# Performance work log

Hardware: AMD Instinct MI355X
Metric: run time of the kernel (lower is better)

Reference implementation:

```python
import jax, jax.numpy as jnp
import numpy as np

N = 131072          # flattened ray-sample points
C = 32              # output_coordinate_dim per plane
BASE = 128          # base grid resolution
SCALES = [1, 2, 4]  # multiscale_res multipliers
HID = 256           # ResBlock / CondMLP hidden width
OUT = 16            # decoder output dim (geo features)
COMBS = [(0, 1), (0, 2), (1, 2)]  # itertools.combinations(range(3), 2)


def setup_inputs() -> dict:
    key = jax.random.key(0)
    ks = iter(jax.random.split(key, 64))
    inp = {}
    inp['pts'] = jax.random.uniform(next(ks), (N, 3), dtype=jnp.float32)
    inp['aabb'] = jnp.asarray([[0.0, 0.0, 0.0], [1.0, 1.0, 1.0]], dtype=jnp.float32)
    # 9 plane grids: 3 scales x 3 coordinate combinations, uniform in [0.1, 0.5)
    for s, mult in enumerate(SCALES):
        r = BASE * mult
        for ci in range(3):
            inp[f'plane_{s}_{ci}'] = jax.random.uniform(
                next(ks), (C, r, r), dtype=jnp.float32, minval=0.1, maxval=0.5)
    feat_dim = C * len(SCALES)  # concat across scales -> 96
    def lin(k, fin, fout):
        bound = 1.0 / np.sqrt(fin)
        kw, kb = jax.random.split(k)
        w = jax.random.uniform(kw, (fin, fout), dtype=jnp.float32, minval=-bound, maxval=bound)
        b = jax.random.uniform(kb, (fout,), dtype=jnp.float32, minval=-bound, maxval=bound)
        return w, b
    inp['l0_w'], inp['l0_b'] = lin(next(ks), feat_dim, HID)
    # 3 ResBlocks x 3 linears (lz, l1, l2), all 256x256 -> stacked
    rw, rb = [], []
    for _ in range(9):
        w, b = lin(next(ks), HID, HID)
        rw.append(w); rb.append(b)
    inp['res_w'] = jnp.stack(rw).reshape(3, 3, HID, HID)
    inp['res_b'] = jnp.stack(rb).reshape(3, 3, HID)
    inp['l1_w'], inp['l1_b'] = lin(next(ks), HID, OUT)
    return inp


def _bilinear(plane, xy):
    # plane: [C, H, W]; xy: [N, 2] in [-1, 1]; x -> W axis, y -> H axis
    # (F.grid_sample, align_corners=True; border clamp == zeros pad since pts in-bounds)
    Cc, H, W = plane.shape
    x = (xy[:, 0] + 1.0) * 0.5 * (W - 1)
    y = (xy[:, 1] + 1.0) * 0.5 * (H - 1)
    x0 = jnp.clip(jnp.floor(x), 0, W - 2).astype(jnp.int32)
    y0 = jnp.clip(jnp.floor(y), 0, H - 2).astype(jnp.int32)
    x1, y1 = x0 + 1, y0 + 1
    wx = (x - x0)[None, :]
    wy = (y - y0)[None, :]
    v = (plane[:, y0, x0] * (1 - wx) * (1 - wy)
         + plane[:, y0, x1] * wx * (1 - wy)
         + plane[:, y1, x0] * (1 - wx) * wy
         + plane[:, y1, x1] * wx * wy)          # [C, N]
    return v.T                                   # [N, C]


def _interp_ms(xn, planes):
    # planes: list of 3 scales, each a list of 3 [C,H,W] grids
    feats = []
    for scale_planes in planes:
        interp = 1.0
        for plane, (c0, c1) in zip(scale_planes, COMBS):
            xy = jnp.stack([xn[:, c0], xn[:, c1]], axis=-1)
            interp = interp * _bilinear(plane, xy)  # hadamard across planes
        feats.append(interp)
    return jnp.concatenate(feats, axis=-1)          # [N, C*num_scales]


def _cond_mlp(f, l0_w, l0_b, res_w, res_b, l1_w, l1_b):
    x = f @ l0_w + l0_b
    for i in range(3):
        z = jax.nn.relu(x @ res_w[i, 0] + res_b[i, 0])
        res = x + z
        x = jax.nn.relu(res @ res_w[i, 1] + res_b[i, 1])
        x = jax.nn.relu(x @ res_w[i, 2] + res_b[i, 2]) + res
    return jax.nn.sigmoid(x @ l1_w + l1_b)


def reference(pts, aabb,
              plane_0_0, plane_0_1, plane_0_2,
              plane_1_0, plane_1_1, plane_1_2,
              plane_2_0, plane_2_1, plane_2_2,
              l0_w, l0_b, res_w, res_b, l1_w, l1_b):
    xn = (pts - aabb[0]) * (2.0 / (aabb[1] - aabb[0])) - 1.0  # normalize_aabb
    planes = [[plane_0_0, plane_0_1, plane_0_2],
              [plane_1_0, plane_1_1, plane_1_2],
              [plane_2_0, plane_2_1, plane_2_2]]
    feats = _interp_ms(xn, planes)                            # [N, 96]
    return _cond_mlp(feats, l0_w, l0_b, res_w, res_b, l1_w, l1_b)  # [N, 16]
```

## Files before the change

kernel.cpp:

```cpp
#include <hip/hip_runtime.h>

typedef unsigned short u16;
typedef unsigned int u32;
typedef __attribute__((ext_vector_type(2))) unsigned int u32x2;
typedef __attribute__((ext_vector_type(8))) short short8;
typedef __attribute__((ext_vector_type(8))) _Float16 half8;
typedef __attribute__((ext_vector_type(2))) __fp16 fp16x2;
typedef __attribute__((ext_vector_type(4))) float floatx4;

__device__ __forceinline__ u16 f2h(float f){ _Float16 h = (_Float16)f; return __builtin_bit_cast(u16, h); }
__device__ __forceinline__ u32 pkrtz(float a, float b){
  fp16x2 h = __builtin_amdgcn_cvt_pkrtz(a, b);
  return __builtin_bit_cast(u32, h);
}
__device__ __forceinline__ u32 pkmax0(u32 a){
  u32 d, z = 0;
  asm("v_pk_max_f16 %0, %1, %2" : "=v"(d) : "v"(a), "v"(z));
  return d;
}
__device__ __forceinline__ u32 pkadd(u32 a, u32 b){
  u32 d;
  asm("v_pk_add_f16 %0, %1, %2" : "=v"(d) : "v"(a), "v"(b));
  return d;
}

struct PlanePtrs { const void* p[9]; };
struct PtransArgs { const float* src[9]; u16* dst[9]; int blk0[10]; int HW[9]; };

__global__ void ptrans_all_kernel(PtransArgs a){
  __shared__ float tile[32][257];
  int bi = blockIdx.x;
  int i = 0;
  #pragma unroll
  for (int k = 1; k < 9; k++) if (bi >= a.blk0[k]) i = k;
  const float* src = a.src[i];
  u16* dst = a.dst[i];
  const int HW = a.HW[i];
  const int t = threadIdx.x;
  const size_t hw0 = (size_t)(bi - a.blk0[i]) * 256;
  #pragma unroll
  for (int c = 0; c < 32; c++) tile[c][t] = src[(size_t)c*HW + hw0 + t];
  __syncthreads();
  u32* d32 = (u32*)(dst + hw0*32);
  #pragma unroll
  for (int k = 0; k < 16; k++){
    int idx = k*512 + t*2;
    int j = idx >> 5, cc = idx & 31;
    u32 lo = f2h(tile[cc][j]);
    u32 hi = f2h(tile[cc+1][j]);
    d32[k*256 + t] = lo | (hi << 16);
  }
}

__device__ __forceinline__ void wconv_one(const float* src, u16* dst, int fin, int fout, int t){
  int per = fin * fout;
  int m = t / per, r = t - m*per;
  int KS = fin >> 5;
  int e = r & 7;
  int lane = (r >> 3) & 63;
  int fs = r >> 9;
  int ks = fs % KS, ft = fs / KS;
  int of = ft*16 + (lane & 15);
  int k  = ks*32 + (lane >> 4)*8 + e;
  dst[t] = f2h(src[(size_t)m*per + (size_t)k*fout + of]);
}
__global__ void wconv_all_kernel(const float* l0_w, const float* res_w, const float* l1_w,
                                 u16* l0T, u16* resT, u16* l1T){
  int t = blockIdx.x*256 + threadIdx.x;
  if (t < 24576){ wconv_one(l0_w, l0T, 96, 256, t); return; }
  t -= 24576;
  if (t < 589824){ wconv_one(res_w, resT, 256, 256, t); return; }
  t -= 589824;
  if (t < 4096){ wconv_one(l1_w, l1T, 256, 16, t); }
}

__device__ __forceinline__ u32 morton_key(const float* __restrict__ pts,
                                          const float* __restrict__ aabb, int n){
  u32 key = 0;
  #pragma unroll
  for (int d=0; d<3; d++){
    float lo = aabb[d], hi = aabb[3+d];
    float xn = (pts[(size_t)n*3 + d] - lo) * (2.0f/(hi - lo)) - 1.0f;
    int q = (int)((xn + 1.0f) * 16.0f);
    q = q < 0 ? 0 : (q > 31 ? 31 : q);
    #pragma unroll
    for (int b=0; b<5; b++) key |= ((u32)(q >> b) & 1u) << (b*3 + d);
  }
  return key;
}
__global__ void hist_zero_kernel(u32* hist){ hist[blockIdx.x*256 + threadIdx.x] = 0; }
__global__ void hist_kernel(const float* pts, const float* aabb, u32* hist, int N){
  int n = blockIdx.x*256 + threadIdx.x;
  if (n >= N) return;
  atomicAdd(&hist[morton_key(pts, aabb, n)], 1u);
}
__global__ void scan_kernel(u32* hist){
  __shared__ u32 sums[1024];
  int t = threadIdx.x;
  u32 local[32]; u32 s = 0;
  #pragma unroll
  for (int i=0; i<32; i++){ local[i] = hist[t*32 + i]; s += local[i]; }
  sums[t] = s;
  __syncthreads();
  for (int off=1; off<1024; off<<=1){
    u32 v = (t >= off) ? sums[t-off] : 0;
    __syncthreads();
    sums[t] += v;
    __syncthreads();
  }
  u32 base = (t == 0) ? 0 : sums[t-1];
  #pragma unroll
  for (int i=0; i<32; i++){ u32 c = local[i]; hist[t*32 + i] = base; base += c; }
}
__global__ void scatter_kernel(const float* pts, const float* aabb, u32* hist,
                               int* sidx, int N){
  int n = blockIdx.x*256 + threadIdx.x;
  if (n >= N) return;
  u32 pos = atomicAdd(&hist[morton_key(pts, aabb, n)], 1u);
  sidx[pos] = n;
}

__global__ void interp_fb_kernel(const float* __restrict__ pts, const float* __restrict__ aabb,
                                 PlanePtrs pp, u16* __restrict__ feats, int N)
{
  int n = blockIdx.x*256 + threadIdx.x;
  if (n >= N) return;
  float xn[3];
  #pragma unroll
  for (int d=0; d<3; d++){
    float lo = aabb[d], hi = aabb[3+d];
    xn[d] = (pts[(size_t)n*3 + d] - lo) * (2.0f/(hi - lo)) - 1.0f;
  }
  const int c0s[3] = {0,0,1};
  const int c1s[3] = {1,2,2};
  #pragma unroll
  for (int s=0; s<3; s++){
    const int R = 128 << s;
    float prod[32];
    #pragma unroll
    for (int p=0; p<3; p++){
      float fx = (xn[c0s[p]] + 1.0f) * 0.5f * (float)(R-1);
      float fy = (xn[c1s[p]] + 1.0f) * 0.5f * (float)(R-1);
      float fx0 = fminf(fmaxf(floorf(fx), 0.0f), (float)(R-2));
      float fy0 = fminf(fmaxf(floorf(fy), 0.0f), (float)(R-2));
      int x0 = (int)fx0, y0 = (int)fy0;
      float wx = fx - fx0, wy = fy - fy0;
      float w00 = (1.0f-wx)*(1.0f-wy), w01 = wx*(1.0f-wy);
      float w10 = (1.0f-wx)*wy,        w11 = wx*wy;
      const size_t HW = (size_t)R*R;
      const float* b00f = (const float*)pp.p[s*3+p] + (size_t)y0*R + x0;
      #pragma unroll 4
      for (int c=0; c<32; c++){
        const float* q = b00f + (size_t)c*HW;
        float val = q[0]*w00 + q[1]*w01 + q[R]*w10 + q[R+1]*w11;
        prod[c] = (p == 0) ? val : prod[c]*val;
      }
    }
    #pragma unroll
    for (int vv=0; vv<4; vv++){
      short8 pk8;
      #pragma unroll
      for (int e=0; e<8; e++) pk8[e] = (short)f2h(prod[vv*8+e]);
      *(short8*)(feats + (size_t)n*96 + s*32 + vv*8) = pk8;
    }
  }
}

template<int KSTEPS>
__device__ __forceinline__ void mm_tile(const u16* X, const u16* __restrict__ WTs,
                                        int ftbase, int lane, const floatx4 binit[4],
                                        floatx4 acc[4][4])
{
  const int lr = lane & 15, lg = lane >> 4;
  #pragma unroll
  for (int rf=0; rf<4; rf++)
    #pragma unroll
    for (int cf=0; cf<4; cf++)
      acc[rf][cf] = binit[rf];
  #pragma unroll 1
  for (int ks=0; ks<KSTEPS; ks++){
    half8 w[4];
    #pragma unroll
    for (int rf=0; rf<4; rf++)
      w[rf] = *(const half8*)(WTs + ((size_t)((ftbase+rf)*KSTEPS + ks)*64 + lane)*8);
    half8 x[4];
    #pragma unroll
    for (int cf=0; cf<4; cf++){
      int pt = cf*16 + lr;
      int byt = (pt*512 + (ks*32 + lg*8)*2) ^ ((pt & 31) << 4);
      x[cf] = *(const half8*)((const char*)X + byt);
    }
    __builtin_amdgcn_s_setprio(1);
    #pragma unroll
    for (int rf=0; rf<4; rf++)
      #pragma unroll
      for (int cf=0; cf<4; cf++)
        acc[rf][cf] = __builtin_amdgcn_mfma_f32_16x16x32_f16(w[rf], x[cf], acc[rf][cf], 0, 0, 0);
    __builtin_amdgcn_s_setprio(0);
  }
}

__device__ __forceinline__ void load_binit(const float* b, int wb, int lg, floatx4* bi){
  #pragma unroll
  for (int rf=0; rf<4; rf++){
    float4 v = *(const float4*)(b + wb + rf*16 + lg*4);
    bi[rf] = (floatx4){v.x, v.y, v.z, v.w};
  }
}

template<int MODE>
__global__ __launch_bounds__(256, 3) void mlp_kernel(
    const float* __restrict__ pts, const float* __restrict__ aabb, PlanePtrs pp,
    const u16* __restrict__ feats, const int* __restrict__ sidx,
    const u16* __restrict__ l0T, const u16* __restrict__ resT, const u16* __restrict__ l1T,
    const float* __restrict__ l0_b, const float* __restrict__ res_b, const float* __restrict__ l1_b,
    float* __restrict__ out)
{
  __shared__ u16 X[64*256];
  const int tid = threadIdx.x;
  const int wave = tid >> 6, lane = tid & 63;
  const int lr = lane & 15, lg = lane >> 4;
  int bid = blockIdx.x;
  if constexpr (MODE == 2){
    int nwg = gridDim.x;
    if ((nwg & 7) == 0) bid = (bid & 7)*(nwg >> 3) + (bid >> 3);
  }
  const int n0 = bid * 64;
  const int ftbase = wave * 4;
  const int wb = wave * 64;

  if constexpr (MODE >= 1){
    const int pt = tid >> 2, v = tid & 3;
    const int n = (MODE == 2) ? sidx[n0 + pt] : (n0 + pt);
    float xn[3];
    #pragma unroll
    for (int d=0; d<3; d++){
      float lo = aabb[d], hi = aabb[3+d];
      xn[d] = (pts[(size_t)n*3 + d] - lo) * (2.0f/(hi - lo)) - 1.0f;
    }
    const int c0s[3] = {0,0,1};
    const int c1s[3] = {1,2,2};
    #pragma unroll
    for (int s=0; s<3; s++){
      const int R = 128 << s;
      float prod[8];
      #pragma unroll
      for (int p=0; p<3; p++){
        float fx = (xn[c0s[p]] + 1.0f) * 0.5f * (float)(R-1);
        float fy = (xn[c1s[p]] + 1.0f) * 0.5f * (float)(R-1);
        float fx0 = fminf(fmaxf(floorf(fx), 0.0f), (float)(R-2));
        float fy0 = fminf(fmaxf(floorf(fy), 0.0f), (float)(R-2));
        int x0 = (int)fx0, y0 = (int)fy0;
        float wx = fx - fx0, wy = fy - fy0;
        float w00 = (1.0f-wx)*(1.0f-wy), w01 = wx*(1.0f-wy);
        float w10 = (1.0f-wx)*wy,        w11 = wx*wy;
        const u16* base = (const u16*)pp.p[s*3 + p];
        const u16* b00 = base + ((size_t)y0*R + x0)*32 + v*8;
        const u16* b10 = b00 + (size_t)R*32;
        half8 h00 = *(const half8*)b00;
        half8 h01 = *(const half8*)(b00 + 32);
        half8 h10 = *(const half8*)b10;
        half8 h11 = *(const half8*)(b10 + 32);
        #pragma unroll
        for (int e=0; e<8; e++){
          float val = (float)h00[e]*w00 + (float)h01[e]*w01 + (float)h10[e]*w10 + (float)h11[e]*w11;
          prod[e] = (p == 0) ? val : prod[e]*val;
        }
      }
      short8 pk8;
      #pragma unroll
      for (int e=0; e<8; e++) pk8[e] = (short)f2h(prod[e]);
      int byt = (pt*512 + (s*32 + v*8)*2) ^ ((pt & 31) << 4);
      *(short8*)((char*)X + byt) = pk8;
    }
  } else {
    #pragma unroll
    for (int i=0; i<3; i++){
      int id = tid + i*256;
      int row = id / 12, sub = id - row*12;
      short8 v = *(const short8*)(feats + (size_t)(n0+row)*96 + sub*8);
      int byt = (row*512 + sub*16) ^ ((row & 31) << 4);
      *(short8*)((char*)X + byt) = v;
    }
  }
  __syncthreads();

  floatx4 acc[4][4];
  floatx4 binit[4];
  u32 pk[4][4][2];

  load_binit(l0_b, wb, lg, binit);
  mm_tile<3>(X, l0T, ftbase, lane, binit, acc);
  __syncthreads();
  #pragma unroll
  for (int rf=0; rf<4; rf++){
    int fby = (wb + rf*16 + lg*4)*2;
    #pragma unroll
    for (int cf=0; cf<4; cf++){
      int pt = cf*16 + lr;
      u32 p0 = pkrtz(acc[rf][cf][0], acc[rf][cf][1]);
      u32 p1 = pkrtz(acc[rf][cf][2], acc[rf][cf][3]);
      pk[rf][cf][0] = p0; pk[rf][cf][1] = p1;
      int byt = (pt*512 + fby) ^ ((pt & 31) << 4);
      *(u32x2*)((char*)X + byt) = (u32x2){p0, p1};
    }
  }
  __syncthreads();

  for (int rb=0; rb<3; rb++){
    const u16* W0 = resT + (size_t)(rb*3+0)*65536;
    const u16* W1 = resT + (size_t)(rb*3+1)*65536;
    const u16* W2 = resT + (size_t)(rb*3+2)*65536;
    const float* b0 = res_b + (rb*3+0)*256;
    const float* b1 = res_b + (rb*3+1)*256;
    const float* b2 = res_b + (rb*3+2)*256;

    load_binit(b0, wb, lg, binit);
    mm_tile<8>(X, W0, ftbase, lane, binit, acc);
    __syncthreads();
    #pragma unroll
    for (int rf=0; rf<4; rf++){
      int fby = (wb + rf*16 + lg*4)*2;
      #pragma unroll
      for (int cf=0; cf<4; cf++){
        int pt = cf*16 + lr;
        u32 p0 = pkadd(pk[rf][cf][0], pkmax0(pkrtz(acc[rf][cf][0], acc[rf][cf][1])));
        u32 p1 = pkadd(pk[rf][cf][1], pkmax0(pkrtz(acc[rf][cf][2], acc[rf][cf][3])));
        pk[rf][cf][0] = p0; pk[rf][cf][1] = p1;
        int byt = (pt*512 + fby) ^ ((pt & 31) << 4);
        *(u32x2*)((char*)X + byt) = (u32x2){p0, p1};
      }
    }
    __syncthreads();

    load_binit(b1, wb, lg, binit);
    mm_tile<8>(X, W1, ftbase, lane, binit, acc);
    __syncthreads();
    #pragma unroll
    for (int rf=0; rf<4; rf++){
      int fby = (wb + rf*16 + lg*4)*2;
      #pragma unroll
      for (int cf=0; cf<4; cf++){
        int pt = cf*16 + lr;
        u32 p0 = pkmax0(pkrtz(acc[rf][cf][0], acc[rf][cf][1]));
        u32 p1 = pkmax0(pkrtz(acc[rf][cf][2], acc[rf][cf][3]));
        int byt = (pt*512 + fby) ^ ((pt & 31) << 4);
        *(u32x2*)((char*)X + byt) = (u32x2){p0, p1};
      }
    }
    __syncthreads();

    load_binit(b2, wb, lg, binit);
    mm_tile<8>(X, W2, ftbase, lane, binit, acc);
    __syncthreads();
    #pragma unroll
    for (int rf=0; rf<4; rf++){
      int fby = (wb + rf*16 + lg*4)*2;
      #pragma unroll
      for (int cf=0; cf<4; cf++){
        int pt = cf*16 + lr;
        u32 p0 = pkadd(pkmax0(pkrtz(acc[rf][cf][0], acc[rf][cf][1])), pk[rf][cf][0]);
        u32 p1 = pkadd(pkmax0(pkrtz(acc[rf][cf][2], acc[rf][cf][3])), pk[rf][cf][1]);
        pk[rf][cf][0] = p0; pk[rf][cf][1] = p1;
        int byt = (pt*512 + fby) ^ ((pt & 31) << 4);
        *(u32x2*)((char*)X + byt) = (u32x2){p0, p1};
      }
    }
    __syncthreads();
  }

  floatx4 accf;
  {
    float4 bo = *(const float4*)(l1_b + lg*4);
    accf = (floatx4){bo.x, bo.y, bo.z, bo.w};
  }
  #pragma unroll 1
  for (int ks=0; ks<8; ks++){
    int pt = wave*16 + lr;
    int byt = (pt*512 + (ks*32 + lg*8)*2) ^ ((pt&31)<<4);
    half8 x = *(const half8*)((const char*)X + byt);
    half8 w = *(const half8*)(l1T + ((size_t)ks*64 + lane)*8);
    accf = __builtin_amdgcn_mfma_f32_16x16x32_f16(w, x, accf, 0, 0, 0);
  }
  {
    int li = n0 + wave*16 + lr;
    int n_out = (MODE == 2) ? sidx[li] : li;
    float4 o;
    o.x = 1.0f / (1.0f + __expf(-accf[0]));
    o.y = 1.0f / (1.0f + __expf(-accf[1]));
    o.z = 1.0f / (1.0f + __expf(-accf[2]));
    o.w = 1.0f / (1.0f + __expf(-accf[3]));
    *(float4*)(out + (size_t)n_out*16 + lg*4) = o;
  }
}

extern "C" void kernel_launch(void* const* d_in, const int* in_sizes, int n_in,
                              void* d_out, int out_size, void* d_ws, size_t ws_size,
                              hipStream_t stream)
{
  const float* pts  = (const float*)d_in[0];
  const float* aabb = (const float*)d_in[1];
  const float* l0_w = (const float*)d_in[11];
  const float* res_w= (const float*)d_in[13];
  const float* l1_w = (const float*)d_in[15];
  const float* l0_b = (const float*)d_in[12];
  const float* res_b= (const float*)d_in[14];
  const float* l1_b = (const float*)d_in[16];
  const int N = in_sizes[0] / 3;

  char* ws = (char*)d_ws;
  const size_t woff_l0  = 0;
  const size_t woff_res = 49152;
  const size_t woff_l1  = woff_res + 9*65536*2;
  const size_t foff     = woff_l1 + 8192;
  const size_t poff     = foff + (size_t)N*96*2;

  static const int HWs[3] = {128*128, 256*256, 512*512};
  size_t pel[9]; size_t tot = 0;
  for (int s=0;s<3;s++) for (int p=0;p<3;p++){ pel[s*3+p] = tot; tot += (size_t)HWs[s]*32; }

  const size_t hoff = (poff + tot*2 + 255) & ~(size_t)255;
  const size_t ioff = hoff + 32768*4;
  const bool tr_mode   = (ws_size >= poff + tot*2);
  const bool sort_mode = (ws_size >= ioff + (size_t)N*4) && ((N/64) % 8 == 0) && (N % 256 == 0);

  wconv_all_kernel<<<(24576+589824+4096+255)/256, 256, 0, stream>>>(
      l0_w, res_w, l1_w, (u16*)(ws+woff_l0), (u16*)(ws+woff_res), (u16*)(ws+woff_l1));

  PlanePtrs pp;
  if (tr_mode){
    u16* pbase = (u16*)(ws + poff);
    PtransArgs pa;
    int b0 = 0;
    for (int i=0;i<9;i++){
      int s = i/3;
      pa.src[i] = (const float*)d_in[2+i];
      pa.dst[i] = pbase + pel[i];
      pa.blk0[i] = b0;
      pa.HW[i] = HWs[s];
      b0 += HWs[s]/256;
      pp.p[i] = pbase + pel[i];
    }
    pa.blk0[9] = b0;
    ptrans_all_kernel<<<b0, 256, 0, stream>>>(pa);

    if (sort_mode){
      u32* hist = (u32*)(ws + hoff);
      int* sidx = (int*)(ws + ioff);
      hist_zero_kernel<<<128, 256, 0, stream>>>(hist);
      hist_kernel<<<(N+255)/256, 256, 0, stream>>>(pts, aabb, hist, N);
      scan_kernel<<<1, 1024, 0, stream>>>(hist);
      scatter_kernel<<<(N+255)/256, 256, 0, stream>>>(pts, aabb, hist, sidx, N);
      mlp_kernel<2><<<N/64, 256, 0, stream>>>(pts, aabb, pp, (const u16*)nullptr, sidx,
          (const u16*)(ws+woff_l0), (const u16*)(ws+woff_res), (const u16*)(ws+woff_l1),
          l0_b, res_b, l1_b, (float*)d_out);
    } else {
      mlp_kernel<1><<<N/64, 256, 0, stream>>>(pts, aabb, pp, (const u16*)nullptr, (const int*)nullptr,
          (const u16*)(ws+woff_l0), (const u16*)(ws+woff_res), (const u16*)(ws+woff_l1),
          l0_b, res_b, l1_b, (float*)d_out);
    }
  } else {
    for (int i=0;i<9;i++) pp.p[i] = d_in[2+i];
    interp_fb_kernel<<<(N+255)/256, 256, 0, stream>>>(pts, aabb, pp, (u16*)(ws+foff), N);
    mlp_kernel<0><<<N/64, 256, 0, stream>>>(pts, aabb, pp, (const u16*)(ws+foff), (const int*)nullptr,
        (const u16*)(ws+woff_l0), (const u16*)(ws+woff_res), (const u16*)(ws+woff_l1),
        l0_b, res_b, l1_b, (float*)d_out);
  }
}
```

Measured before the change: 234.8 us.

## Use packed fp16 bilinear interpolation and coarser 12-bit Morton sort

Bilinear weighting and the cross-plane Hadamard product now use packed fp16 multiply and FMA instructions instead of per-element fp32 conversion and arithmetic, which removes the convert instructions and halves the ALU work in the interpolation stage. The Morton sort key drops from 15 to 12 bits, so the histogram and scan shrink from 32768 to 4096 bins. The zero kernel is replaced with hipMemsetAsync. The fp16 accumulation lowers interpolation precision, and the coarser sort may reduce gather locality.

```diff
diff --git a/kernel.cpp b/kernel.cpp
--- a/kernel.cpp
+++ b/kernel.cpp
@@ -3,6 +3,7 @@
 typedef unsigned short u16;
 typedef unsigned int u32;
 typedef __attribute__((ext_vector_type(2))) unsigned int u32x2;
+typedef __attribute__((ext_vector_type(4))) unsigned int u32x4;
 typedef __attribute__((ext_vector_type(8))) short short8;
 typedef __attribute__((ext_vector_type(8))) _Float16 half8;
 typedef __attribute__((ext_vector_type(2))) __fp16 fp16x2;
@@ -21,6 +22,16 @@
 __device__ __forceinline__ u32 pkadd(u32 a, u32 b){
   u32 d;
   asm("v_pk_add_f16 %0, %1, %2" : "=v"(d) : "v"(a), "v"(b));
+  return d;
+}
+__device__ __forceinline__ u32 pkmul(u32 a, u32 b){
+  u32 d;
+  asm("v_pk_mul_f16 %0, %1, %2" : "=v"(d) : "v"(a), "v"(b));
+  return d;
+}
+__device__ __forceinline__ u32 pkfma(u32 a, u32 b, u32 c){
+  u32 d;
+  asm("v_pk_fma_f16 %0, %1, %2, %3" : "=v"(d) : "v"(a), "v"(b), "v"(c));
   return d;
 }
 
@@ -81,14 +92,13 @@
   for (int d=0; d<3; d++){
     float lo = aabb[d], hi = aabb[3+d];
     float xn = (pts[(size_t)n*3 + d] - lo) * (2.0f/(hi - lo)) - 1.0f;
-    int q = (int)((xn + 1.0f) * 16.0f);
-    q = q < 0 ? 0 : (q > 31 ? 31 : q);
-    #pragma unroll
-    for (int b=0; b<5; b++) key |= ((u32)(q >> b) & 1u) << (b*3 + d);
+    int q = (int)((xn + 1.0f) * 8.0f);
+    q = q < 0 ? 0 : (q > 15 ? 15 : q);
+    #pragma unroll
+    for (int b=0; b<4; b++) key |= ((u32)(q >> b) & 1u) << (b*3 + d);
   }
   return key;
 }
-__global__ void hist_zero_kernel(u32* hist){ hist[blockIdx.x*256 + threadIdx.x] = 0; }
 __global__ void hist_kernel(const float* pts, const float* aabb, u32* hist, int N){
   int n = blockIdx.x*256 + threadIdx.x;
   if (n >= N) return;
@@ -97,9 +107,9 @@
 __global__ void scan_kernel(u32* hist){
   __shared__ u32 sums[1024];
   int t = threadIdx.x;
-  u32 local[32]; u32 s = 0;
-  #pragma unroll
-  for (int i=0; i<32; i++){ local[i] = hist[t*32 + i]; s += local[i]; }
+  u32 local[4]; u32 s = 0;
+  #pragma unroll
+  for (int i=0; i<4; i++){ local[i] = hist[t*4 + i]; s += local[i]; }
   sums[t] = s;
   __syncthreads();
   for (int off=1; off<1024; off<<=1){
@@ -110,7 +120,7 @@
   }
   u32 base = (t == 0) ? 0 : sums[t-1];
   #pragma unroll
-  for (int i=0; i<32; i++){ u32 c = local[i]; hist[t*32 + i] = base; base += c; }
+  for (int i=0; i<4; i++){ u32 c = local[i]; hist[t*4 + i] = base; base += c; }
 }
 __global__ void scatter_kernel(const float* pts, const float* aabb, u32* hist,
                                int* sidx, int N){
@@ -243,7 +253,7 @@
     #pragma unroll
     for (int s=0; s<3; s++){
       const int R = 128 << s;
-      float prod[8];
+      u32x4 prod;
       #pragma unroll
       for (int p=0; p<3; p++){
         float fx = (xn[c0s[p]] + 1.0f) * 0.5f * (float)(R-1);
@@ -252,26 +262,28 @@
         float fy0 = fminf(fmaxf(floorf(fy), 0.0f), (float)(R-2));
         int x0 = (int)fx0, y0 = (int)fy0;
         float wx = fx - fx0, wy = fy - fy0;
-        float w00 = (1.0f-wx)*(1.0f-wy), w01 = wx*(1.0f-wy);
-        float w10 = (1.0f-wx)*wy,        w11 = wx*wy;
+        u32 w00p = pkrtz((1.0f-wx)*(1.0f-wy), (1.0f-wx)*(1.0f-wy));
+        u32 w01p = pkrtz(wx*(1.0f-wy),        wx*(1.0f-wy));
+        u32 w10p = pkrtz((1.0f-wx)*wy,        (1.0f-wx)*wy);
+        u32 w11p = pkrtz(wx*wy,               wx*wy);
         const u16* base = (const u16*)pp.p[s*3 + p];
         const u16* b00 = base + ((size_t)y0*R + x0)*32 + v*8;
         const u16* b10 = b00 + (size_t)R*32;
-        half8 h00 = *(const half8*)b00;
-        half8 h01 = *(const half8*)(b00 + 32);
-        half8 h10 = *(const half8*)b10;
-        half8 h11 = *(const half8*)(b10 + 32);
+        u32x4 h00 = *(const u32x4*)b00;
+        u32x4 h01 = *(const u32x4*)(b00 + 32);
+        u32x4 h10 = *(const u32x4*)b10;
+        u32x4 h11 = *(const u32x4*)(b10 + 32);
         #pragma unroll
-        for (int e=0; e<8; e++){
-          float val = (float)h00[e]*w00 + (float)h01[e]*w01 + (float)h10[e]*w10 + (float)h11[e]*w11;
-          prod[e] = (p == 0) ? val : prod[e]*val;
+        for (int i=0; i<4; i++){
+          u32 a = pkmul(h00[i], w00p);
+          a = pkfma(h01[i], w01p, a);
+          a = pkfma(h10[i], w10p, a);
+          a = pkfma(h11[i], w11p, a);
+          prod[i] = (p == 0) ? a : pkmul(prod[i], a);
         }
       }
-      short8 pk8;
-      #pragma unroll
-      for (int e=0; e<8; e++) pk8[e] = (short)f2h(prod[e]);
       int byt = (pt*512 + (s*32 + v*8)*2) ^ ((pt & 31) << 4);
-      *(short8*)((char*)X + byt) = pk8;
+      *(u32x4*)((char*)X + byt) = prod;
     }
   } else {
     #pragma unroll
@@ -420,7 +432,7 @@
   for (int s=0;s<3;s++) for (int p=0;p<3;p++){ pel[s*3+p] = tot; tot += (size_t)HWs[s]*32; }
 
   const size_t hoff = (poff + tot*2 + 255) & ~(size_t)255;
-  const size_t ioff = hoff + 32768*4;
+  const size_t ioff = hoff + 4096*4;
   const bool tr_mode   = (ws_size >= poff + tot*2);
   const bool sort_mode = (ws_size >= ioff + (size_t)N*4) && ((N/64) % 8 == 0) && (N % 256 == 0);
 
@@ -447,7 +459,7 @@
     if (sort_mode){
       u32* hist = (u32*)(ws + hoff);
       int* sidx = (int*)(ws + ioff);
-      hist_zero_kernel<<<128, 256, 0, stream>>>(hist);
+      hipMemsetAsync(hist, 0, 4096*4, stream);
       hist_kernel<<<(N+255)/256, 256, 0, stream>>>(pts, aabb, hist, N);
       scan_kernel<<<1, 1024, 0, stream>>>(hist);
       scatter_kernel<<<(N+255)/256, 256, 0, stream>>>(pts, aabb, hist, sidx, N);
```

Measured after the change: 235.5 us. Within noise of the previous version (+0.3%).
